# Performance work log

Measured on AMD Instinct MI355X. Metric: run time of the kernel, lower is better.

Reference implementation:

```python
import jax, jax.numpy as jnp
import numpy as np

N_NODES = 100000
N_EDGES = 300000
D_IN = 256
D_OUT = 256


def setup_inputs() -> dict:
    key = jax.random.key(0)
    k1, k2, k3 = jax.random.split(key, 3)
    z = jax.random.normal(k1, (N_NODES, D_IN), dtype=jnp.float32)
    edge_index = jax.random.randint(k2, (2, N_EDGES), 0, N_NODES, dtype=jnp.int64)
    # Linear(input_dim, out_dim): weight [out, in], stored transposed for x @ W
    W = jax.random.normal(k3, (D_IN, D_OUT), dtype=jnp.float32) / np.sqrt(D_IN)
    b = jnp.zeros((D_OUT,), dtype=jnp.float32)
    return {"z": z, "edge_index": edge_index, "W": W, "b": b}


def reference(z, edge_index, W, b):
    # h = Linear(z): [N, D_out]
    h = z @ W + b
    # gather endpoint embeddings and take per-edge dot product
    src = h[edge_index[0]]  # [E, D_out]
    dst = h[edge_index[1]]  # [E, D_out]
    value = jnp.sum(src * dst, axis=1)  # [E]
    return jax.nn.sigmoid(value)
```

## Files before the change

kernel.cpp:

```cpp
#include <hip/hip_runtime.h>
#include <hip/hip_bf16.h>
#include <hip/hip_fp16.h>
#include <math.h>


#define D_DIM 256
#define BM 128

typedef __attribute__((ext_vector_type(8))) short bf16x8;
typedef __attribute__((ext_vector_type(4))) float f32x4;

__device__ bf16x8 g_Wh[8 * 256 * 4];
__device__ bf16x8 g_Wl[8 * 256 * 4];

__device__ inline unsigned short bf16_rn(float x) {
  unsigned u = __builtin_bit_cast(unsigned, x);
  unsigned r = u + 0x7FFFu + ((u >> 16) & 1u);
  return (unsigned short)(r >> 16);
}
__device__ inline float bf16_f(unsigned short s) {
  return __builtin_bit_cast(float, (unsigned)s << 16);
}

__device__ inline void split8(const float4 f0, const float4 f1, bf16x8& hi, bf16x8& lo) {
  float v[8] = {f0.x, f0.y, f0.z, f0.w, f1.x, f1.y, f1.z, f1.w};
#pragma unroll
  for (int j = 0; j < 8; j++) {
    unsigned short hb = bf16_rn(v[j]);
    hi[j] = (short)hb;
    lo[j] = (short)bf16_rn(v[j] - bf16_f(hb));
  }
}

__global__ __launch_bounds__(256) void pack_w_kernel(const float* __restrict__ W) {
  int t = blockIdx.x * 256 + threadIdx.x;
  int kb = t >> 10;
  int qd = (t >> 8) & 3;
  int n  = t & 255;
  float v[8];
#pragma unroll
  for (int j = 0; j < 8; j++)
    v[j] = W[(size_t)(kb * 32 + qd * 8 + j) * D_DIM + n];
  bf16x8 hi, lo;
  split8(make_float4(v[0], v[1], v[2], v[3]),
         make_float4(v[4], v[5], v[6], v[7]), hi, lo);
  int fi = (kb * 256 + n) * 4 + qd;
  g_Wh[fi] = hi;
  g_Wl[fi] = lo;
}

__device__ inline void stage_b(int kb, char* buf, int wv, int lane) {
  const char* gsrc = (wv < 4)
      ? ((const char*)g_Wh + (size_t)kb * 16384 + (wv & 3) * 4096)
      : ((const char*)g_Wl + (size_t)kb * 16384 + (wv & 3) * 4096);
  char* ldst = buf + ((wv < 4) ? 0 : 16384) + (wv & 3) * 4096;
#pragma unroll
  for (int i = 0; i < 4; i++) {
    __builtin_amdgcn_global_load_lds(
        (const __attribute__((address_space(1))) void*)(gsrc + i * 1024 + lane * 16),
        (__attribute__((address_space(3))) void*)(ldst + i * 1024),
        16, 0, 0);
  }
}

__global__ __launch_bounds__(512) void gemm_mfma_kernel(
    const float* __restrict__ z, const float* __restrict__ b,
    __half* __restrict__ h, int nrows) {
  __shared__ char smem[2 * 32768];
  const int tid = threadIdx.x;
  const int lane = tid & 63;
  const int wv = tid >> 6;
  const int mg = wv >> 1;
  const int nh = wv & 1;
  const int fr = lane & 15;
  const int qd = lane >> 4;
  const int row0 = blockIdx.x * BM + mg * 32;

  f32x4 acc[2][8];
#pragma unroll
  for (int i = 0; i < 2; i++)
#pragma unroll
    for (int j = 0; j < 8; j++) acc[i][j] = (f32x4)0.f;

  const float* zp[2];
#pragma unroll
  for (int fm = 0; fm < 2; fm++) {
    int r = row0 + fm * 16 + fr;
    r = r < nrows ? r : (nrows - 1);
    zp[fm] = z + (size_t)r * D_DIM + qd * 8;
  }

  float4 a0[2], a1[2];
#pragma unroll
  for (int fm = 0; fm < 2; fm++) {
    a0[fm] = *(const float4*)(zp[fm]);
    a1[fm] = *(const float4*)(zp[fm] + 4);
  }
  stage_b(0, smem, wv, lane);
  __syncthreads();

#pragma unroll 2
  for (int kb = 0; kb < 8; kb++) {
    char* cur = smem + (kb & 1) * 32768;
    if (kb < 7) stage_b(kb + 1, smem + ((kb + 1) & 1) * 32768, wv, lane);

    bf16x8 ah[2], al[2];
#pragma unroll
    for (int fm = 0; fm < 2; fm++) split8(a0[fm], a1[fm], ah[fm], al[fm]);
    if (kb < 7) {
#pragma unroll
      for (int fm = 0; fm < 2; fm++) {
        const float* p = zp[fm] + (kb + 1) * 32;
        a0[fm] = *(const float4*)(p);
        a1[fm] = *(const float4*)(p + 4);
      }
    }

    const bf16x8* bufh = (const bf16x8*)cur;
    const bf16x8* bufl = (const bf16x8*)(cur + 16384);
#pragma unroll
    for (int fn = 0; fn < 8; fn++) {
      int fi = (nh * 128 + fn * 16 + fr) * 4 + qd;
      bf16x8 bh = bufh[fi];
      bf16x8 bl = bufl[fi];
#pragma unroll
      for (int fm = 0; fm < 2; fm++) {
        acc[fm][fn] = __builtin_amdgcn_mfma_f32_16x16x32_bf16(ah[fm], bh, acc[fm][fn], 0, 0, 0);
        acc[fm][fn] = __builtin_amdgcn_mfma_f32_16x16x32_bf16(ah[fm], bl, acc[fm][fn], 0, 0, 0);
        acc[fm][fn] = __builtin_amdgcn_mfma_f32_16x16x32_bf16(al[fm], bh, acc[fm][fn], 0, 0, 0);
      }
    }
    __syncthreads();
  }

  __half* et = (__half*)(smem + wv * 4096);
  float bias[8];
#pragma unroll
  for (int fn = 0; fn < 8; fn++) bias[fn] = b[nh * 128 + fn * 16 + fr];

#pragma unroll
  for (int fm = 0; fm < 2; fm++) {
#pragma unroll
    for (int fn = 0; fn < 8; fn++)
#pragma unroll
      for (int r = 0; r < 4; r++)
        et[(qd * 4 + r) * 128 + fn * 16 + fr] = __float2half(acc[fm][fn][r] + bias[fn]);
#pragma unroll
    for (int p = 0; p < 4; p++) {
      int idx = p * 64 + lane;
      int rr = idx >> 4;
      int cc = idx & 15;
      float4 v = *(const float4*)(et + rr * 128 + cc * 8);
      int row = row0 + fm * 16 + rr;
      if (row < nrows)
        *(float4*)(h + (size_t)row * D_DIM + nh * 128 + cc * 8) = v;
    }
  }
}

__global__ __launch_bounds__(256) void edge_dot_kernel(
    const int* __restrict__ ei, const __half* __restrict__ h,
    float* __restrict__ out, int E) {
  int gid = blockIdx.x * blockDim.x + threadIdx.x;
  int g = gid >> 4;
  int lane = gid & 15;
  int ebase = g * 4;
  if (ebase >= E) return;

  float4 sv[4][2], dv[4][2];
  int ec[4];
#pragma unroll
  for (int q = 0; q < 4; q++) {
    int e = ebase + q;
    ec[q] = e < E ? e : (E - 1);
  }
#pragma unroll
  for (int q = 0; q < 4; q++) {
    int s = ei[ec[q]];
    int d = ei[E + ec[q]];
    const float4* sp = (const float4*)(h + (size_t)s * D_DIM);
    const float4* dp = (const float4*)(h + (size_t)d * D_DIM);
#pragma unroll
    for (int c = 0; c < 2; c++) {
      sv[q][c] = sp[c * 16 + lane];
      dv[q][c] = dp[c * 16 + lane];
    }
  }
  float acc[4] = {0.f, 0.f, 0.f, 0.f};
#pragma unroll
  for (int q = 0; q < 4; q++) {
#pragma unroll
    for (int c = 0; c < 2; c++) {
      const __half2* s2 = (const __half2*)&sv[q][c];
      const __half2* d2 = (const __half2*)&dv[q][c];
#pragma unroll
      for (int j = 0; j < 4; j++) {
        float2 a = __half22float2(s2[j]);
        float2 b2 = __half22float2(d2[j]);
        acc[q] += a.x * b2.x + a.y * b2.y;
      }
    }
  }
#pragma unroll
  for (int m = 1; m <= 8; m <<= 1) {
#pragma unroll
    for (int q = 0; q < 4; q++) acc[q] += __shfl_xor(acc[q], m);
  }
  if (lane == 0) {
    if (ebase + 3 < E) {
      float4 o;
      o.x = 1.0f / (1.0f + expf(-acc[0]));
      o.y = 1.0f / (1.0f + expf(-acc[1]));
      o.z = 1.0f / (1.0f + expf(-acc[2]));
      o.w = 1.0f / (1.0f + expf(-acc[3]));
      *(float4*)(out + ebase) = o;
    } else {
#pragma unroll
      for (int q = 0; q < 4; q++)
        if (ebase + q < E) out[ebase + q] = 1.0f / (1.0f + expf(-acc[q]));
    }
  }
}

extern "C" void kernel_launch(void* const* d_in, const int* in_sizes, int n_in,
                              void* d_out, int out_size, void* d_ws, size_t ws_size,
                              hipStream_t stream) {
  const float* z  = (const float*)d_in[0];
  const int*   ei = (const int*)d_in[1];
  const float* W  = (const float*)d_in[2];
  const float* b  = (const float*)d_in[3];
  float* out = (float*)d_out;
  __half* h  = (__half*)d_ws;

  const int nnodes = in_sizes[0] / D_DIM;
  const int E = in_sizes[1] / 2;

  pack_w_kernel<<<32, 256, 0, stream>>>(W);

  dim3 grid_gemm((nnodes + BM - 1) / BM);
  gemm_mfma_kernel<<<grid_gemm, 512, 0, stream>>>(z, b, h, nnodes);

  int groups = (E + 3) / 4;
  dim3 grid_edge(((size_t)groups * 16 + 255) / 256);
  edge_dot_kernel<<<grid_edge, 256, 0, stream>>>(ei, h, out, E);
}
```

Baseline: 248.0 us.

## Pad GEMM epilogue LDS tile and restructure edge-dot to wave-per-8-edges

```diff
diff --git a/kernel.cpp b/kernel.cpp
--- a/kernel.cpp
+++ b/kernel.cpp
@@ -133,7 +133,7 @@
     __syncthreads();
   }
 
-  __half* et = (__half*)(smem + wv * 4096);
+  __half* et = (__half*)(smem + wv * 4608);
   float bias[8];
 #pragma unroll
   for (int fn = 0; fn < 8; fn++) bias[fn] = b[nh * 128 + fn * 16 + fr];
@@ -144,13 +144,13 @@
     for (int fn = 0; fn < 8; fn++)
 #pragma unroll
       for (int r = 0; r < 4; r++)
-        et[(qd * 4 + r) * 128 + fn * 16 + fr] = __float2half(acc[fm][fn][r] + bias[fn]);
+        et[(qd * 4 + r) * 136 + fn * 16 + fr] = __float2half(acc[fm][fn][r] + bias[fn]);
 #pragma unroll
     for (int p = 0; p < 4; p++) {
       int idx = p * 64 + lane;
       int rr = idx >> 4;
       int cc = idx & 15;
-      float4 v = *(const float4*)(et + rr * 128 + cc * 8);
+      float4 v = *(const float4*)(et + rr * 136 + cc * 8);
       int row = row0 + fm * 16 + rr;
       if (row < nrows)
         *(float4*)(h + (size_t)row * D_DIM + nh * 128 + cc * 8) = v;
@@ -161,64 +161,46 @@
 __global__ __launch_bounds__(256) void edge_dot_kernel(
     const int* __restrict__ ei, const __half* __restrict__ h,
     float* __restrict__ out, int E) {
-  int gid = blockIdx.x * blockDim.x + threadIdx.x;
-  int g = gid >> 4;
-  int lane = gid & 15;
-  int ebase = g * 4;
+  int wid = (blockIdx.x * blockDim.x + threadIdx.x) >> 6;
+  int lane = threadIdx.x & 63;
+  int ebase = wid * 8;
   if (ebase >= E) return;
-
-  float4 sv[4][2], dv[4][2];
-  int ec[4];
-#pragma unroll
-  for (int q = 0; q < 4; q++) {
+  const int half = lane >> 5;
+  const int off = lane & 31;
+
+  float4 v[8];
+#pragma unroll
+  for (int q = 0; q < 8; q++) {
     int e = ebase + q;
-    ec[q] = e < E ? e : (E - 1);
-  }
-#pragma unroll
-  for (int q = 0; q < 4; q++) {
-    int s = ei[ec[q]];
-    int d = ei[E + ec[q]];
-    const float4* sp = (const float4*)(h + (size_t)s * D_DIM);
-    const float4* dp = (const float4*)(h + (size_t)d * D_DIM);
-#pragma unroll
-    for (int c = 0; c < 2; c++) {
-      sv[q][c] = sp[c * 16 + lane];
-      dv[q][c] = dp[c * 16 + lane];
-    }
-  }
-  float acc[4] = {0.f, 0.f, 0.f, 0.f};
-#pragma unroll
-  for (int q = 0; q < 4; q++) {
-#pragma unroll
-    for (int c = 0; c < 2; c++) {
-      const __half2* s2 = (const __half2*)&sv[q][c];
-      const __half2* d2 = (const __half2*)&dv[q][c];
-#pragma unroll
-      for (int j = 0; j < 4; j++) {
-        float2 a = __half22float2(s2[j]);
-        float2 b2 = __half22float2(d2[j]);
-        acc[q] += a.x * b2.x + a.y * b2.y;
-      }
-    }
-  }
-#pragma unroll
-  for (int m = 1; m <= 8; m <<= 1) {
-#pragma unroll
-    for (int q = 0; q < 4; q++) acc[q] += __shfl_xor(acc[q], m);
-  }
-  if (lane == 0) {
-    if (ebase + 3 < E) {
-      float4 o;
-      o.x = 1.0f / (1.0f + expf(-acc[0]));
-      o.y = 1.0f / (1.0f + expf(-acc[1]));
-      o.z = 1.0f / (1.0f + expf(-acc[2]));
-      o.w = 1.0f / (1.0f + expf(-acc[3]));
-      *(float4*)(out + ebase) = o;
-    } else {
-#pragma unroll
-      for (int q = 0; q < 4; q++)
-        if (ebase + q < E) out[ebase + q] = 1.0f / (1.0f + expf(-acc[q]));
-    }
+    e = e < E ? e : (E - 1);
+    int node = half ? ei[E + e] : ei[e];
+    v[q] = *(const float4*)((const __half*)h + (size_t)node * D_DIM + off * 8);
+  }
+
+  float res = 0.f;
+#pragma unroll
+  for (int q = 0; q < 8; q++) {
+    float4 w;
+    w.x = __shfl_xor(v[q].x, 32);
+    w.y = __shfl_xor(v[q].y, 32);
+    w.z = __shfl_xor(v[q].z, 32);
+    w.w = __shfl_xor(v[q].w, 32);
+    const __half2* a2 = (const __half2*)&v[q];
+    const __half2* b2 = (const __half2*)&w;
+    float part = 0.f;
+#pragma unroll
+    for (int j = 0; j < 4; j++) {
+      float2 fa = __half22float2(a2[j]);
+      float2 fb = __half22float2(b2[j]);
+      part += fa.x * fb.x + fa.y * fb.y;
+    }
+#pragma unroll
+    for (int m = 1; m <= 16; m <<= 1) part += __shfl_xor(part, m);
+    res = (lane == q) ? part : res;
+  }
+  if (lane < 8) {
+    int e = ebase + lane;
+    if (e < E) out[e] = 1.0f / (1.0f + __expf(-res));
   }
 }
 
@@ -240,7 +222,7 @@
   dim3 grid_gemm((nnodes + BM - 1) / BM);
   gemm_mfma_kernel<<<grid_gemm, 512, 0, stream>>>(z, b, h, nnodes);
 
-  int groups = (E + 3) / 4;
-  dim3 grid_edge(((size_t)groups * 16 + 255) / 256);
+  int waves = (E + 7) / 8;
+  dim3 grid_edge(((size_t)waves * 64 + 255) / 256);
   edge_dot_kernel<<<grid_edge, 256, 0, stream>>>(ei, h, out, E);
 }
```

Measured after the change: 246.1 us. About the same (-0.8%).
